# Performance work log

Hardware: AMD Instinct MI355X
Metric: run time of the kernel (lower is better)

The kernel has to match this reference:

```python
import jax, jax.numpy as jnp
import numpy as np

N, C_IN, C_RED, H, W = 16, 256, 64, 48, 48


def conv1x1(x, w, b):
    # x: [N, Cin, H, W], w: [Cout, Cin], b: [Cout]
    return jnp.einsum('nchw,oc->nohw', x, w) + b[None, :, None, None]


def setup_inputs() -> dict:
    key = jax.random.key(0)
    ks = jax.random.split(key, 10)
    s_in = 1.0 / np.sqrt(C_IN)
    s_red = 1.0 / np.sqrt(C_RED)
    return {
        'feature_maps': jax.random.normal(ks[0], (N, C_IN, H, W), jnp.float32),
        'global_channel_output': jax.random.normal(ks[1], (N, C_IN, H, W), jnp.float32),
        'Wq': jax.random.uniform(ks[2], (C_RED, C_IN), jnp.float32, -s_in, s_in),
        'bq': jax.random.uniform(ks[3], (C_RED,), jnp.float32, -s_in, s_in),
        'Wk': jax.random.uniform(ks[4], (C_RED, C_IN), jnp.float32, -s_in, s_in),
        'bk': jax.random.uniform(ks[5], (C_RED,), jnp.float32, -s_in, s_in),
        'Wv': jax.random.uniform(ks[6], (C_RED, C_IN), jnp.float32, -s_in, s_in),
        'bv': jax.random.uniform(ks[7], (C_RED,), jnp.float32, -s_in, s_in),
        'Watt': jax.random.uniform(ks[8], (C_IN, C_RED), jnp.float32, -s_red, s_red),
        'batt': jax.random.uniform(ks[9], (C_IN,), jnp.float32, -s_red, s_red),
    }


def reference(feature_maps, global_channel_output, Wq, bq, Wk, bk, Wv, bv, Watt, batt):
    n, _, h, w = feature_maps.shape
    hw = h * w
    q = conv1x1(feature_maps, Wq, bq).reshape(n, -1, hw)   # [N, Cr, HW]
    k = conv1x1(feature_maps, Wk, bk).reshape(n, -1, hw)   # [N, Cr, HW]
    v = conv1x1(feature_maps, Wv, bv).reshape(n, -1, hw)   # [N, Cr, HW]
    # key^T @ query -> [N, HW, HW]
    qk = jnp.einsum('nci,ncj->nij', k, q)
    # global (flattened) softmax over the whole HWxHW matrix per batch element
    qk = jax.nn.softmax(qk.reshape(n, hw * hw), axis=-1).reshape(n, hw, hw)
    att = jnp.einsum('nci,nij->ncj', v, qk).reshape(n, -1, h, w)  # [N, Cr, H, W]
    att = conv1x1(att, Watt, batt)                                 # [N, Cin, H, W]
    return global_channel_output * att + global_channel_output
```

## Files before the change

### kernel.cpp

```cpp
#include <hip/hip_runtime.h>
#include <hip/hip_bf16.h>
#include <stdint.h>

#define NB   16
#define CIN  256
#define CRED 64
#define HW   2304
#define NJT  36
#define NIG  2
#define NIT  18

typedef __bf16 bf16;
typedef __bf16 bf16x8 __attribute__((ext_vector_type(8)));
typedef __bf16 bf16x4 __attribute__((ext_vector_type(4)));
typedef float  f32x4  __attribute__((ext_vector_type(4)));

__global__ __launch_bounds__(256) void prep_kernel(
    const float* __restrict__ Wq, const float* __restrict__ bq,
    const float* __restrict__ Wk, const float* __restrict__ Wv,
    const float* __restrict__ Watt,
    bf16* __restrict__ Wqb, bf16* __restrict__ Wkb, bf16* __restrict__ Wvb,
    bf16* __restrict__ Wab, float* __restrict__ bqs)
{
    const float INVLN2 = 1.44269504088896f;
    int i = blockIdx.x * 256 + threadIdx.x;
    Wqb[i] = (bf16)(Wq[i] * INVLN2);
    Wkb[i] = (bf16)Wk[i];
    Wvb[i] = (bf16)Wv[i];
    Wab[i] = (bf16)Watt[i];
    if (i < CRED) bqs[i] = bq[i] * INVLN2;
}

__global__ __launch_bounds__(256) void qkv_kernel(
    const float* __restrict__ x,
    const bf16* __restrict__ Wqb, const float* __restrict__ bqs,
    const bf16* __restrict__ Wkb, const float* __restrict__ bk,
    const bf16* __restrict__ Wvb, const float* __restrict__ bv,
    bf16* __restrict__ qT, bf16* __restrict__ kT, bf16* __restrict__ v)
{
    __shared__ __align__(16) bf16 sX[32 * 264];
    const int jt = blockIdx.x, n = blockIdx.y;
    const int jbase = jt * 32;
    const int tid = threadIdx.x;
    const int lane = tid & 63, w = tid >> 6;
    const int l15 = lane & 15, q4 = lane >> 4;

    const float* xn = x + ((size_t)n * CIN) * HW + jbase;
    #pragma unroll
    for (int it = 0; it < 8; ++it) {
        int idx = tid + 256 * it;
        int c = idx >> 3, p4 = idx & 7;
        const float4 vv = *(const float4*)(xn + c * HW + p4 * 4);
        sX[(p4 * 4 + 0) * 264 + c] = (bf16)vv.x;
        sX[(p4 * 4 + 1) * 264 + c] = (bf16)vv.y;
        sX[(p4 * 4 + 2) * 264 + c] = (bf16)vv.z;
        sX[(p4 * 4 + 3) * 264 + c] = (bf16)vv.w;
    }
    __syncthreads();

    const bf16*  Ws[3] = {Wqb, Wkb, Wvb};
    const float* bs[3] = {bqs, bk, bv};
    #pragma unroll
    for (int wi = 0; wi < 3; ++wi) {
        bf16x8 a[8];
        const bf16* Wp = Ws[wi] + (w * 16 + l15) * CIN + q4 * 8;
        #pragma unroll
        for (int ks = 0; ks < 8; ++ks) a[ks] = *(const bf16x8*)(Wp + ks * 32);
        f32x4 acc[2] = {};
        #pragma unroll
        for (int nt = 0; nt < 2; ++nt) {
            #pragma unroll
            for (int ks = 0; ks < 8; ++ks) {
                bf16x8 b = *(const bf16x8*)(sX + (nt * 16 + l15) * 264 + ks * 32 + q4 * 8);
                acc[nt] = __builtin_amdgcn_mfma_f32_16x16x32_bf16(a[ks], b, acc[nt], 0, 0, 0);
            }
        }
        const int crb = w * 16 + q4 * 4;
        const float b0 = bs[wi][crb], b1 = bs[wi][crb + 1],
                    b2 = bs[wi][crb + 2], b3 = bs[wi][crb + 3];
        if (wi < 2) {
            bf16* dst = (wi == 0 ? qT : kT) + ((size_t)n * HW) * 64;
            #pragma unroll
            for (int nt = 0; nt < 2; ++nt) {
                int pos = jbase + nt * 16 + l15;
                bf16x4 pk = {(bf16)(acc[nt].x + b0), (bf16)(acc[nt].y + b1),
                             (bf16)(acc[nt].z + b2), (bf16)(acc[nt].w + b3)};
                *(bf16x4*)(dst + pos * 64 + crb) = pk;
            }
        } else {
            bf16* dst = v + ((size_t)n * CRED) * HW;
            #pragma unroll
            for (int nt = 0; nt < 2; ++nt) {
                int pos = jbase + nt * 16 + l15;
                dst[(crb + 0) * HW + pos] = (bf16)(acc[nt].x + b0);
                dst[(crb + 1) * HW + pos] = (bf16)(acc[nt].y + b1);
                dst[(crb + 2) * HW + pos] = (bf16)(acc[nt].z + b2);
                dst[(crb + 3) * HW + pos] = (bf16)(acc[nt].w + b3);
            }
        }
    }
}

__global__ __launch_bounds__(256, 4) void attn_kernel(
    const bf16* __restrict__ qT, const bf16* __restrict__ kT,
    const bf16* __restrict__ v,
    float* __restrict__ OTp, float* __restrict__ Z)
{
    __shared__ __align__(16) bf16 sQP[64 * 72];
    __shared__ __align__(16) bf16 sK[64 * 72];
    __shared__ __align__(16) bf16 sV[64 * 72];
    const int jt = blockIdx.x, ig = blockIdx.y, n = blockIdx.z;
    const int jbase = jt * 64;
    const int tid = threadIdx.x;
    const int lane = tid & 63, w = tid >> 6;
    const int l15 = lane & 15, q4 = lane >> 4;

    {
        const uint4* src = (const uint4*)(qT + ((size_t)n * HW + jbase) * 64);
        uint4* dst = (uint4*)sQP;
        for (int i = tid; i < 512; i += 256) {
            int r = i >> 3, c = i & 7;
            dst[r * 9 + c] = src[r * 8 + c];
        }
    }
    __syncthreads();
    bf16x8 qf[4][2];
    #pragma unroll
    for (int nt = 0; nt < 4; ++nt)
        #pragma unroll
        for (int ks = 0; ks < 2; ++ks)
            qf[nt][ks] = *(const bf16x8*)(sQP + (nt * 16 + l15) * 72 + ks * 32 + q4 * 8);

    f32x4 oacc[4] = {};
    float zacc = 0.f;
    const uint4* ksrc = (const uint4*)(kT + ((size_t)n * HW) * 64);
    const bf16* vbase = v + ((size_t)n * CRED) * HW;

    const int r0 = tid >> 3, c0 = tid & 7;
    const int ibase0 = ig * NIT * 64;

    uint4 kr0 = ksrc[(ibase0 + r0) * 8 + c0];
    uint4 kr1 = ksrc[(ibase0 + r0 + 32) * 8 + c0];
    uint4 vr0 = *(const uint4*)(vbase + (size_t)r0 * HW + ibase0 + c0 * 8);
    uint4 vr1 = *(const uint4*)(vbase + (size_t)(r0 + 32) * HW + ibase0 + c0 * 8);

    uint4* dk = (uint4*)sK;
    uint4* dv = (uint4*)sV;

    for (int it = 0; it < NIT; ++it) {
        const int ibase = ibase0 + it * 64;
        __syncthreads();
        dk[r0 * 9 + c0] = kr0;
        dk[(r0 + 32) * 9 + c0] = kr1;
        dv[r0 * 9 + c0] = vr0;
        dv[(r0 + 32) * 9 + c0] = vr1;
        const int nbase = (it + 1 < NIT) ? ibase + 64 : ibase;
        kr0 = ksrc[(nbase + r0) * 8 + c0];
        kr1 = ksrc[(nbase + r0 + 32) * 8 + c0];
        vr0 = *(const uint4*)(vbase + (size_t)r0 * HW + nbase + c0 * 8);
        vr1 = *(const uint4*)(vbase + (size_t)(r0 + 32) * HW + nbase + c0 * 8);
        __syncthreads();

        bf16x8 kf0 = *(const bf16x8*)(sK + (w * 16 + l15) * 72 + 0 * 32 + q4 * 8);
        bf16x8 kf1 = *(const bf16x8*)(sK + (w * 16 + l15) * 72 + 1 * 32 + q4 * 8);
        #pragma unroll
        for (int nt = 0; nt < 4; ++nt) {
            f32x4 accs = {};
            accs = __builtin_amdgcn_mfma_f32_16x16x32_bf16(kf0, qf[nt][0], accs, 0, 0, 0);
            accs = __builtin_amdgcn_mfma_f32_16x16x32_bf16(kf1, qf[nt][1], accs, 0, 0, 0);
            float p0 = exp2f(accs.x), p1 = exp2f(accs.y);
            float p2 = exp2f(accs.z), p3 = exp2f(accs.w);
            zacc += (p0 + p1) + (p2 + p3);
            bf16x4 pk = {(bf16)p0, (bf16)p1, (bf16)p2, (bf16)p3};
            *(bf16x4*)(sQP + (nt * 16 + l15) * 72 + w * 16 + q4 * 4) = pk;
        }
        __syncthreads();
        bf16x8 vf0 = *(const bf16x8*)(sV + (w * 16 + l15) * 72 + 0 * 32 + q4 * 8);
        bf16x8 vf1 = *(const bf16x8*)(sV + (w * 16 + l15) * 72 + 1 * 32 + q4 * 8);
        #pragma unroll
        for (int nt = 0; nt < 4; ++nt) {
            bf16x8 p0 = *(const bf16x8*)(sQP + (nt * 16 + l15) * 72 + 0 * 32 + q4 * 8);
            bf16x8 p1 = *(const bf16x8*)(sQP + (nt * 16 + l15) * 72 + 1 * 32 + q4 * 8);
            oacc[nt] = __builtin_amdgcn_mfma_f32_16x16x32_bf16(vf0, p0, oacc[nt], 0, 0, 0);
            oacc[nt] = __builtin_amdgcn_mfma_f32_16x16x32_bf16(vf1, p1, oacc[nt], 0, 0, 0);
        }
    }
    float* OTn = OTp + (((size_t)ig * NB + n) * HW) * 64;
    #pragma unroll
    for (int nt = 0; nt < 4; ++nt) {
        int pos = jbase + nt * 16 + l15;
        *(f32x4*)(OTn + pos * 64 + w * 16 + q4 * 4) = oacc[nt];
    }
    #pragma unroll
    for (int off = 32; off > 0; off >>= 1) zacc += __shfl_down(zacc, off);
    if (lane == 0) atomicAdd(Z + n, zacc);
}

__global__ __launch_bounds__(256) void out_kernel(
    const float* __restrict__ OTp, const float* __restrict__ Z,
    const bf16* __restrict__ Wab, const float* __restrict__ batt,
    const float* __restrict__ g, float* __restrict__ out)
{
    __shared__ __align__(16) bf16 sO[64 * 72];
    const int jt = blockIdx.x, n = blockIdx.y;
    const int jbase = jt * 64;
    const int tid = threadIdx.x;
    const int lane = tid & 63, w = tid >> 6;
    const int l15 = lane & 15, q4 = lane >> 4;
    const float invZ = 1.0f / Z[n];

    for (int i = tid; i < 1024; i += 256) {
        int r = i >> 4, c4 = i & 15;
        const float* p = OTp + (((size_t)n * HW) + jbase + r) * 64 + c4 * 4;
        float4 v0 = *(const float4*)(p);
        float4 v1 = *(const float4*)(p + (size_t)NB * HW * 64);
        bf16x4 pk = {(bf16)((v0.x + v1.x) * invZ),
                     (bf16)((v0.y + v1.y) * invZ),
                     (bf16)((v0.z + v1.z) * invZ),
                     (bf16)((v0.w + v1.w) * invZ)};
        *(bf16x4*)(sO + r * 72 + c4 * 4) = pk;
    }
    __syncthreads();

    bf16x8 bfr[4][2];
    #pragma unroll
    for (int nt = 0; nt < 4; ++nt)
        #pragma unroll
        for (int ks = 0; ks < 2; ++ks)
            bfr[nt][ks] = *(const bf16x8*)(sO + (nt * 16 + l15) * 72 + ks * 32 + q4 * 8);

    const float* gp = g + ((size_t)n * CIN) * HW;
    float* op = out + ((size_t)n * CIN) * HW;
    #pragma unroll
    for (int mt = 0; mt < 4; ++mt) {
        const bf16* Wp = Wab + (w * 64 + mt * 16 + l15) * 64 + q4 * 8;
        bf16x8 a0 = *(const bf16x8*)(Wp);
        bf16x8 a1 = *(const bf16x8*)(Wp + 32);
        const int co = w * 64 + mt * 16 + q4 * 4;
        const float c0 = batt[co], c1 = batt[co + 1], c2 = batt[co + 2], c3 = batt[co + 3];
        #pragma unroll
        for (int nt = 0; nt < 4; ++nt) {
            f32x4 acc = {};
            acc = __builtin_amdgcn_mfma_f32_16x16x32_bf16(a0, bfr[nt][0], acc, 0, 0, 0);
            acc = __builtin_amdgcn_mfma_f32_16x16x32_bf16(a1, bfr[nt][1], acc, 0, 0, 0);
            const int pos = jbase + nt * 16 + l15;
            const float g0 = gp[(co + 0) * HW + pos], g1 = gp[(co + 1) * HW + pos];
            const float g2 = gp[(co + 2) * HW + pos], g3 = gp[(co + 3) * HW + pos];
            op[(co + 0) * HW + pos] = g0 * (acc.x + c0 + 1.0f);
            op[(co + 1) * HW + pos] = g1 * (acc.y + c1 + 1.0f);
            op[(co + 2) * HW + pos] = g2 * (acc.z + c2 + 1.0f);
            op[(co + 3) * HW + pos] = g3 * (acc.w + c3 + 1.0f);
        }
    }
}

extern "C" void kernel_launch(void* const* d_in, const int* in_sizes, int n_in,
                              void* d_out, int out_size, void* d_ws, size_t ws_size,
                              hipStream_t stream) {
    const float* x    = (const float*)d_in[0];
    const float* g    = (const float*)d_in[1];
    const float* Wq   = (const float*)d_in[2];
    const float* bq   = (const float*)d_in[3];
    const float* Wk   = (const float*)d_in[4];
    const float* bk   = (const float*)d_in[5];
    const float* Wv   = (const float*)d_in[6];
    const float* bv   = (const float*)d_in[7];
    const float* Watt = (const float*)d_in[8];
    const float* batt = (const float*)d_in[9];
    float* out = (float*)d_out;

    char* ws = (char*)d_ws;
    const size_t qkv_sz = (size_t)NB * HW * CRED * sizeof(bf16);
    bf16*  qT  = (bf16*)(ws);
    bf16*  kT  = (bf16*)(ws + qkv_sz);
    bf16*  vv  = (bf16*)(ws + 2 * qkv_sz);
    float* OTp = (float*)(ws + 3 * qkv_sz);
    char*  w2  = ws + 3 * qkv_sz + (size_t)NIG * NB * HW * CRED * sizeof(float);
    float* Zp  = (float*)(w2);
    bf16*  Wqb = (bf16*)(w2 + 256);
    bf16*  Wkb = Wqb + CRED * CIN;
    bf16*  Wvb = Wkb + CRED * CIN;
    bf16*  Wab = Wvb + CRED * CIN;
    float* bqs = (float*)(Wab + CIN * CRED);

    hipMemsetAsync(Zp, 0, NB * sizeof(float), stream);

    dim3 blk(256);
    prep_kernel<<<dim3(64), blk, 0, stream>>>(Wq, bq, Wk, Wv, Watt, Wqb, Wkb, Wvb, Wab, bqs);
    qkv_kernel<<<dim3(HW / 32, NB), blk, 0, stream>>>(x, Wqb, bqs, Wkb, bk, Wvb, bv, qT, kT, vv);
    attn_kernel<<<dim3(NJT, NIG, NB), blk, 0, stream>>>(qT, kT, vv, OTp, Zp);
    out_kernel<<<dim3(NJT, NB), blk, 0, stream>>>(OTp, Zp, Wab, batt, g, out);
}
```

Before: 251.4 us.

## Widen attention blocks to 512 threads, split keys four ways, store partials in bf16

The attention kernel now uses 512-thread blocks covering 128 query columns. Two wave groups share each staged K/V tile, and the key range is split into four groups instead of two. The register prefetch of the next K/V tile is removed, so global loads are no longer overlapped with compute. Partial outputs are written in bf16 rather than fp32. The output kernel sums the four partials with extra MFMAs over the reduction dimension, applies 1/Z after the matmul, and uses 32-column tiles with preloaded weights. The aim is more K/V reuse per load and less partial-output traffic, at the cost of bf16 rounding in the partials and lost load/compute overlap.

```diff
diff --git a/kernel.cpp b/kernel.cpp
--- a/kernel.cpp
+++ b/kernel.cpp
@@ -6,9 +6,8 @@
 #define CIN  256
 #define CRED 64
 #define HW   2304
-#define NJT  36
-#define NIG  2
-#define NIT  18
+#define NIG  4
+#define NIT  9
 
 typedef __bf16 bf16;
 typedef __bf16 bf16x8 __attribute__((ext_vector_type(8)));
@@ -101,24 +100,27 @@
     }
 }
 
-__global__ __launch_bounds__(256, 4) void attn_kernel(
+__global__ __launch_bounds__(512, 8) void attn_kernel(
     const bf16* __restrict__ qT, const bf16* __restrict__ kT,
     const bf16* __restrict__ v,
-    float* __restrict__ OTp, float* __restrict__ Z)
-{
-    __shared__ __align__(16) bf16 sQP[64 * 72];
+    bf16* __restrict__ OTp, float* __restrict__ Z)
+{
+    __shared__ __align__(16) bf16 sP[128 * 72];
     __shared__ __align__(16) bf16 sK[64 * 72];
     __shared__ __align__(16) bf16 sV[64 * 72];
     const int jt = blockIdx.x, ig = blockIdx.y, n = blockIdx.z;
-    const int jbase = jt * 64;
+    const int jbase = jt * 128;
     const int tid = threadIdx.x;
     const int lane = tid & 63, w = tid >> 6;
     const int l15 = lane & 15, q4 = lane >> 4;
+    const int wi = w & 3;
+    const int jh = w >> 2;
 
     {
         const uint4* src = (const uint4*)(qT + ((size_t)n * HW + jbase) * 64);
-        uint4* dst = (uint4*)sQP;
-        for (int i = tid; i < 512; i += 256) {
+        uint4* dst = (uint4*)sP;
+        #pragma unroll
+        for (int i = tid; i < 1024; i += 512) {
             int r = i >> 3, c = i & 7;
             dst[r * 9 + c] = src[r * 8 + c];
         }
@@ -129,40 +131,23 @@
     for (int nt = 0; nt < 4; ++nt)
         #pragma unroll
         for (int ks = 0; ks < 2; ++ks)
-            qf[nt][ks] = *(const bf16x8*)(sQP + (nt * 16 + l15) * 72 + ks * 32 + q4 * 8);
+            qf[nt][ks] = *(const bf16x8*)(sP + (jh * 64 + nt * 16 + l15) * 72 + ks * 32 + q4 * 8);
 
     f32x4 oacc[4] = {};
     float zacc = 0.f;
     const uint4* ksrc = (const uint4*)(kT + ((size_t)n * HW) * 64);
     const bf16* vbase = v + ((size_t)n * CRED) * HW;
-
     const int r0 = tid >> 3, c0 = tid & 7;
-    const int ibase0 = ig * NIT * 64;
-
-    uint4 kr0 = ksrc[(ibase0 + r0) * 8 + c0];
-    uint4 kr1 = ksrc[(ibase0 + r0 + 32) * 8 + c0];
-    uint4 vr0 = *(const uint4*)(vbase + (size_t)r0 * HW + ibase0 + c0 * 8);
-    uint4 vr1 = *(const uint4*)(vbase + (size_t)(r0 + 32) * HW + ibase0 + c0 * 8);
-
-    uint4* dk = (uint4*)sK;
-    uint4* dv = (uint4*)sV;
 
     for (int it = 0; it < NIT; ++it) {
-        const int ibase = ibase0 + it * 64;
+        const int ibase = (ig * NIT + it) * 64;
         __syncthreads();
-        dk[r0 * 9 + c0] = kr0;
-        dk[(r0 + 32) * 9 + c0] = kr1;
-        dv[r0 * 9 + c0] = vr0;
-        dv[(r0 + 32) * 9 + c0] = vr1;
-        const int nbase = (it + 1 < NIT) ? ibase + 64 : ibase;
-        kr0 = ksrc[(nbase + r0) * 8 + c0];
-        kr1 = ksrc[(nbase + r0 + 32) * 8 + c0];
-        vr0 = *(const uint4*)(vbase + (size_t)r0 * HW + nbase + c0 * 8);
-        vr1 = *(const uint4*)(vbase + (size_t)(r0 + 32) * HW + nbase + c0 * 8);
+        ((uint4*)sK)[r0 * 9 + c0] = ksrc[(ibase + r0) * 8 + c0];
+        ((uint4*)sV)[r0 * 9 + c0] = *(const uint4*)(vbase + (size_t)r0 * HW + ibase + c0 * 8);
         __syncthreads();
 
-        bf16x8 kf0 = *(const bf16x8*)(sK + (w * 16 + l15) * 72 + 0 * 32 + q4 * 8);
-        bf16x8 kf1 = *(const bf16x8*)(sK + (w * 16 + l15) * 72 + 1 * 32 + q4 * 8);
+        bf16x8 kf0 = *(const bf16x8*)(sK + (wi * 16 + l15) * 72 + q4 * 8);
+        bf16x8 kf1 = *(const bf16x8*)(sK + (wi * 16 + l15) * 72 + 32 + q4 * 8);
         #pragma unroll
         for (int nt = 0; nt < 4; ++nt) {
             f32x4 accs = {};
@@ -172,24 +157,25 @@
             float p2 = exp2f(accs.z), p3 = exp2f(accs.w);
             zacc += (p0 + p1) + (p2 + p3);
             bf16x4 pk = {(bf16)p0, (bf16)p1, (bf16)p2, (bf16)p3};
-            *(bf16x4*)(sQP + (nt * 16 + l15) * 72 + w * 16 + q4 * 4) = pk;
+            *(bf16x4*)(sP + (jh * 64 + nt * 16 + l15) * 72 + wi * 16 + q4 * 4) = pk;
         }
         __syncthreads();
-        bf16x8 vf0 = *(const bf16x8*)(sV + (w * 16 + l15) * 72 + 0 * 32 + q4 * 8);
-        bf16x8 vf1 = *(const bf16x8*)(sV + (w * 16 + l15) * 72 + 1 * 32 + q4 * 8);
+        bf16x8 vf0 = *(const bf16x8*)(sV + (wi * 16 + l15) * 72 + q4 * 8);
+        bf16x8 vf1 = *(const bf16x8*)(sV + (wi * 16 + l15) * 72 + 32 + q4 * 8);
         #pragma unroll
         for (int nt = 0; nt < 4; ++nt) {
-            bf16x8 p0 = *(const bf16x8*)(sQP + (nt * 16 + l15) * 72 + 0 * 32 + q4 * 8);
-            bf16x8 p1 = *(const bf16x8*)(sQP + (nt * 16 + l15) * 72 + 1 * 32 + q4 * 8);
+            bf16x8 p0 = *(const bf16x8*)(sP + (jh * 64 + nt * 16 + l15) * 72 + q4 * 8);
+            bf16x8 p1 = *(const bf16x8*)(sP + (jh * 64 + nt * 16 + l15) * 72 + 32 + q4 * 8);
             oacc[nt] = __builtin_amdgcn_mfma_f32_16x16x32_bf16(vf0, p0, oacc[nt], 0, 0, 0);
             oacc[nt] = __builtin_amdgcn_mfma_f32_16x16x32_bf16(vf1, p1, oacc[nt], 0, 0, 0);
         }
     }
-    float* OTn = OTp + (((size_t)ig * NB + n) * HW) * 64;
+    bf16* OTn = OTp + (((size_t)ig * NB + n) * HW) * 64;
     #pragma unroll
     for (int nt = 0; nt < 4; ++nt) {
-        int pos = jbase + nt * 16 + l15;
-        *(f32x4*)(OTn + pos * 64 + w * 16 + q4 * 4) = oacc[nt];
+        int pos = jbase + jh * 64 + nt * 16 + l15;
+        bf16x4 o = {(bf16)oacc[nt].x, (bf16)oacc[nt].y, (bf16)oacc[nt].z, (bf16)oacc[nt].w};
+        *(bf16x4*)(OTn + pos * 64 + wi * 16 + q4 * 4) = o;
     }
     #pragma unroll
     for (int off = 32; off > 0; off >>= 1) zacc += __shfl_down(zacc, off);
@@ -197,59 +183,66 @@
 }
 
 __global__ __launch_bounds__(256) void out_kernel(
-    const float* __restrict__ OTp, const float* __restrict__ Z,
+    const bf16* __restrict__ OTp, const float* __restrict__ Z,
     const bf16* __restrict__ Wab, const float* __restrict__ batt,
     const float* __restrict__ g, float* __restrict__ out)
 {
-    __shared__ __align__(16) bf16 sO[64 * 72];
+    __shared__ __align__(16) bf16 sO[NIG * 32 * 72];
     const int jt = blockIdx.x, n = blockIdx.y;
-    const int jbase = jt * 64;
+    const int jbase = jt * 32;
     const int tid = threadIdx.x;
     const int lane = tid & 63, w = tid >> 6;
     const int l15 = lane & 15, q4 = lane >> 4;
     const float invZ = 1.0f / Z[n];
 
+    bf16x8 a[4][2];
+    #pragma unroll
+    for (int mt = 0; mt < 4; ++mt)
+        #pragma unroll
+        for (int ks = 0; ks < 2; ++ks)
+            a[mt][ks] = *(const bf16x8*)(Wab + (w * 64 + mt * 16 + l15) * 64 + ks * 32 + q4 * 8);
+
+    #pragma unroll
     for (int i = tid; i < 1024; i += 256) {
-        int r = i >> 4, c4 = i & 15;
-        const float* p = OTp + (((size_t)n * HW) + jbase + r) * 64 + c4 * 4;
-        float4 v0 = *(const float4*)(p);
-        float4 v1 = *(const float4*)(p + (size_t)NB * HW * 64);
-        bf16x4 pk = {(bf16)((v0.x + v1.x) * invZ),
-                     (bf16)((v0.y + v1.y) * invZ),
-                     (bf16)((v0.z + v1.z) * invZ),
-                     (bf16)((v0.w + v1.w) * invZ)};
-        *(bf16x4*)(sO + r * 72 + c4 * 4) = pk;
+        int ig = i >> 8, rem = i & 255, r = rem >> 3, c = rem & 7;
+        ((uint4*)sO)[(ig * 32 + r) * 9 + c] =
+            ((const uint4*)OTp)[(((size_t)ig * NB + n) * HW + jbase + r) * 8 + c];
     }
     __syncthreads();
 
-    bf16x8 bfr[4][2];
-    #pragma unroll
-    for (int nt = 0; nt < 4; ++nt)
-        #pragma unroll
-        for (int ks = 0; ks < 2; ++ks)
-            bfr[nt][ks] = *(const bf16x8*)(sO + (nt * 16 + l15) * 72 + ks * 32 + q4 * 8);
+    f32x4 acc[4][2] = {};
+    #pragma unroll
+    for (int ig = 0; ig < NIG; ++ig) {
+        bf16x8 b[2][2];
+        #pragma unroll
+        for (int nt = 0; nt < 2; ++nt)
+            #pragma unroll
+            for (int ks = 0; ks < 2; ++ks)
+                b[nt][ks] = *(const bf16x8*)(sO + (ig * 32 + nt * 16 + l15) * 72 + ks * 32 + q4 * 8);
+        #pragma unroll
+        for (int mt = 0; mt < 4; ++mt)
+            #pragma unroll
+            for (int nt = 0; nt < 2; ++nt) {
+                acc[mt][nt] = __builtin_amdgcn_mfma_f32_16x16x32_bf16(a[mt][0], b[nt][0], acc[mt][nt], 0, 0, 0);
+                acc[mt][nt] = __builtin_amdgcn_mfma_f32_16x16x32_bf16(a[mt][1], b[nt][1], acc[mt][nt], 0, 0, 0);
+            }
+    }
 
     const float* gp = g + ((size_t)n * CIN) * HW;
     float* op = out + ((size_t)n * CIN) * HW;
     #pragma unroll
     for (int mt = 0; mt < 4; ++mt) {
-        const bf16* Wp = Wab + (w * 64 + mt * 16 + l15) * 64 + q4 * 8;
-        bf16x8 a0 = *(const bf16x8*)(Wp);
-        bf16x8 a1 = *(const bf16x8*)(Wp + 32);
         const int co = w * 64 + mt * 16 + q4 * 4;
         const float c0 = batt[co], c1 = batt[co + 1], c2 = batt[co + 2], c3 = batt[co + 3];
         #pragma unroll
-        for (int nt = 0; nt < 4; ++nt) {
-            f32x4 acc = {};
-            acc = __builtin_amdgcn_mfma_f32_16x16x32_bf16(a0, bfr[nt][0], acc, 0, 0, 0);
-            acc = __builtin_amdgcn_mfma_f32_16x16x32_bf16(a1, bfr[nt][1], acc, 0, 0, 0);
+        for (int nt = 0; nt < 2; ++nt) {
             const int pos = jbase + nt * 16 + l15;
             const float g0 = gp[(co + 0) * HW + pos], g1 = gp[(co + 1) * HW + pos];
             const float g2 = gp[(co + 2) * HW + pos], g3 = gp[(co + 3) * HW + pos];
-            op[(co + 0) * HW + pos] = g0 * (acc.x + c0 + 1.0f);
-            op[(co + 1) * HW + pos] = g1 * (acc.y + c1 + 1.0f);
-            op[(co + 2) * HW + pos] = g2 * (acc.z + c2 + 1.0f);
-            op[(co + 3) * HW + pos] = g3 * (acc.w + c3 + 1.0f);
+            op[(co + 0) * HW + pos] = g0 * (acc[mt][nt].x * invZ + c0 + 1.0f);
+            op[(co + 1) * HW + pos] = g1 * (acc[mt][nt].y * invZ + c1 + 1.0f);
+            op[(co + 2) * HW + pos] = g2 * (acc[mt][nt].z * invZ + c2 + 1.0f);
+            op[(co + 3) * HW + pos] = g3 * (acc[mt][nt].w * invZ + c3 + 1.0f);
         }
     }
 }
@@ -274,8 +267,8 @@
     bf16*  qT  = (bf16*)(ws);
     bf16*  kT  = (bf16*)(ws + qkv_sz);
     bf16*  vv  = (bf16*)(ws + 2 * qkv_sz);
-    float* OTp = (float*)(ws + 3 * qkv_sz);
-    char*  w2  = ws + 3 * qkv_sz + (size_t)NIG * NB * HW * CRED * sizeof(float);
+    bf16*  OTp = (bf16*)(ws + 3 * qkv_sz);
+    char*  w2  = ws + (3 + NIG) * qkv_sz;
     float* Zp  = (float*)(w2);
     bf16*  Wqb = (bf16*)(w2 + 256);
     bf16*  Wkb = Wqb + CRED * CIN;
@@ -285,9 +278,8 @@
 
     hipMemsetAsync(Zp, 0, NB * sizeof(float), stream);
 
-    dim3 blk(256);
-    prep_kernel<<<dim3(64), blk, 0, stream>>>(Wq, bq, Wk, Wv, Watt, Wqb, Wkb, Wvb, Wab, bqs);
-    qkv_kernel<<<dim3(HW / 32, NB), blk, 0, stream>>>(x, Wqb, bqs, Wkb, bk, Wvb, bv, qT, kT, vv);
-    attn_kernel<<<dim3(NJT, NIG, NB), blk, 0, stream>>>(qT, kT, vv, OTp, Zp);
-    out_kernel<<<dim3(NJT, NB), blk, 0, stream>>>(OTp, Zp, Wab, batt, g, out);
-}
+    prep_kernel<<<dim3(64), dim3(256), 0, stream>>>(Wq, bq, Wk, Wv, Watt, Wqb, Wkb, Wvb, Wab, bqs);
+    qkv_kernel<<<dim3(HW / 32, NB), dim3(256), 0, stream>>>(x, Wqb, bqs, Wkb, bk, Wvb, bv, qT, kT, vv);
+    attn_kernel<<<dim3(HW / 128, NIG, NB), dim3(512), 0, stream>>>(qT, kT, vv, OTp, Zp);
+    out_kernel<<<dim3(HW / 32, NB), dim3(256), 0, stream>>>(OTp, Zp, Wab, batt, g, out);
+}
```

Measured after the change: 367.9 us. 1.46x slower.
